# Performance work log

Measured on AMD Instinct MI355X. Metric: run time of the kernel, lower is better.

The kernel has to match this reference:

```python
import jax, jax.numpy as jnp
import numpy as np

B, T, C, H = 2, 2048, 1024, 16  # batch, seq, n_embd, n_head


def setup_inputs() -> dict:
    key = jax.random.key(0)
    k1, k2, k3 = jax.random.split(key, 3)
    scale = 0.02
    return {
        "x": jax.random.normal(k1, (B, T, C), dtype=jnp.float32),
        "W_attn": jax.random.normal(k2, (3 * C, C), dtype=jnp.float32) * scale,
        "b_attn": jnp.zeros((3 * C,), dtype=jnp.float32),
        "W_proj": jax.random.normal(k3, (C, C), dtype=jnp.float32) * scale,
        "b_proj": jnp.zeros((C,), dtype=jnp.float32),
        "alpha": jnp.asarray(1.0, dtype=jnp.float32),
        "beta": jnp.asarray(0.1, dtype=jnp.float32),
        "gamma": jnp.asarray(0.1, dtype=jnp.float32),
    }


def reference(x, W_attn, b_attn, W_proj, b_proj, alpha, beta, gamma):
    Bx, Tx, Cx = x.shape
    d = Cx // H  # head dim
    qkv = x @ W_attn.T + b_attn                      # [B,T,3C]
    q, k, v = jnp.split(qkv, 3, axis=-1)

    def to_heads(t):
        return t.reshape(Bx, Tx, H, d).transpose(0, 2, 1, 3)  # [B,H,T,d]

    q, k, v = to_heads(q), to_heads(k), to_heads(v)

    inv_sqrt_d = jnp.asarray(1.0 / np.sqrt(d), dtype=x.dtype)
    scores = jnp.einsum('bhtd,bhsd->bhts', q, k) * inv_sqrt_d  # [B,H,T,T]

    causal = jnp.tril(jnp.ones((Tx, Tx), dtype=bool))
    scores = jnp.where(causal, scores, -jnp.inf)
    att = jax.nn.softmax(scores, axis=-1)

    # Id buffer = softmax(10000*eye) == identity; MC buffer = softmax(10000*tril)
    # == uniform causal prefix average: MC[i, j<=i] = 1/(i+1).
    id_m = jnp.eye(Tx, dtype=x.dtype)
    mc = causal.astype(x.dtype) / jnp.arange(1, Tx + 1, dtype=x.dtype)[:, None]

    shaped = beta * att + alpha * id_m - gamma * mc  # dropout p=0 -> identity
    y = jnp.einsum('bhts,bhsd->bhtd', shaped, v)     # [B,H,T,d]
    y = y.transpose(0, 2, 1, 3).reshape(Bx, Tx, Cx)
    return y @ W_proj.T + b_proj
```

## Files before the change

### kernel.cpp

```cpp
#include <hip/hip_runtime.h>
#include <stdint.h>

#define Bsz  2
#define Tseq 2048
#define Cemb 1024
#define NH   16
#define HD   64

typedef __attribute__((ext_vector_type(8))) __bf16 bf16x8;
typedef __attribute__((ext_vector_type(4))) float  f32x4;
typedef __attribute__((ext_vector_type(8))) unsigned short u16x8;

#define MFMA16(a, b, c) __builtin_amdgcn_mfma_f32_16x16x32_bf16((a), (b), (c), 0, 0, 0)

__device__ __forceinline__ unsigned short f2bf(float f) {
  union { float f; unsigned int u; } v; v.f = f;
  unsigned int u = v.u;
  u += 0x7fffu + ((u >> 16) & 1u);
  return (unsigned short)(u >> 16);
}
__device__ __forceinline__ unsigned short f2bf_rhu(float f) {
  union { float f; unsigned int u; } v; v.f = f;
  return (unsigned short)((v.u + 0x8000u) >> 16);
}
__device__ __forceinline__ float bf2f(unsigned short h) {
  union { unsigned int u; float f; } v; v.u = ((unsigned int)h) << 16;
  return v.f;
}

typedef __attribute__((address_space(1))) const unsigned int GU;
typedef __attribute__((address_space(3))) unsigned int LU;
__device__ __forceinline__ void load_lds16(const void* g, void* l) {
  __builtin_amdgcn_global_load_lds((GU*)g, (LU*)l, 16, 0, 0);
}

__global__ void cast_bf16_kernel(const float* __restrict__ in,
                                 unsigned short* __restrict__ out, int n) {
  int i = (blockIdx.x * blockDim.x + threadIdx.x) * 4;
  if (i < n) {
    const float4 f = *(const float4*)(in + i);
    ushort4 o;
    o.x = f2bf(f.x); o.y = f2bf(f.y); o.z = f2bf(f.z); o.w = f2bf(f.w);
    *(ushort4*)(out + i) = o;
  }
}

__global__ __launch_bounds__(256) void gemm_qkv_kernel(
    const unsigned short* __restrict__ A,
    const unsigned short* __restrict__ Bw,
    const float* __restrict__ bias,
    unsigned short* __restrict__ qkv) {
  const int K = Cemb;
  __shared__ unsigned short sA[128 * 32];
  __shared__ unsigned short sB[128 * 32];
  const int tid = threadIdx.x;
  const int wave = tid >> 6, lane = tid & 63;
  const int quad = lane >> 4, lrow = lane & 15;
  const int l7 = lrow & 7;
  const int wm = (wave >> 1) * 64, wn = (wave & 1) * 64;
  const int tileM = blockIdx.y * 128, tileN = blockIdx.x * 128;

  f32x4 acc[4][4];
#pragma unroll
  for (int i = 0; i < 4; ++i)
#pragma unroll
    for (int j = 0; j < 4; ++j) acc[i][j] = (f32x4){0.f, 0.f, 0.f, 0.f};

  for (int k0 = 0; k0 < K; k0 += 32) {
    __syncthreads();
#pragma unroll
    for (int s = 0; s < 2; ++s) {
      const int cid = tid + s * 256;
      const int r = cid >> 2, ko = (cid & 3) * 8;
      load_lds16(&A[(size_t)(tileM + r) * K + k0 + ko], &sA[cid * 8]);
      load_lds16(&Bw[(size_t)(tileN + r) * K + k0 + ko], &sB[cid * 8]);
    }
    __syncthreads();
    bf16x8 af[4], bfm[4];
#pragma unroll
    for (int mt = 0; mt < 4; ++mt)
      af[mt] = *(const bf16x8*)&sA[(wm + mt * 16 + lrow) * 32 + quad * 8];
#pragma unroll
    for (int nt = 0; nt < 4; ++nt)
      bfm[nt] = *(const bf16x8*)&sB[(wn + nt * 16 + lrow) * 32 + quad * 8];
#pragma unroll
    for (int mt = 0; mt < 4; ++mt)
#pragma unroll
      for (int nt = 0; nt < 4; ++nt)
        acc[mt][nt] = MFMA16(af[mt], bfm[nt], acc[mt][nt]);
  }

  __syncthreads();
  unsigned short* sEp = sA + wave * 1024;
  float bias_v[4];
#pragma unroll
  for (int nt = 0; nt < 4; ++nt) bias_v[nt] = bias[tileN + wn + nt * 16 + lrow];
  const int gn0 = tileN + wn;
  const int part = gn0 >> 10, h = (gn0 & 1023) >> 6;

#pragma unroll
  for (int mt = 0; mt < 4; ++mt) {
#pragma unroll
    for (int nt = 0; nt < 4; ++nt)
#pragma unroll
      for (int reg = 0; reg < 4; ++reg) {
        const int q = quad * 4 + reg;
        const int ch = (nt * 2 + (lrow >> 3)) ^ (q & 7);
        sEp[q * 64 + ch * 8 + l7] = f2bf(acc[mt][nt][reg] + bias_v[nt]);
      }
    __builtin_amdgcn_wave_barrier();
#pragma unroll
    for (int i = 0; i < 2; ++i) {
      const int c = i * 64 + lane;
      const int r = c >> 3, ch2 = c & 7;
      const u16x8 row = *(const u16x8*)&sEp[r * 64 + ((ch2 ^ (r & 7)) << 3)];
      const int gm = tileM + wm + mt * 16 + r;
      const int bb = gm >> 11, t = gm & 2047;
      *(u16x8*)&qkv[((((size_t)part * Bsz + bb) * NH + h) * Tseq + t) * HD + ch2 * 8] = row;
    }
    __builtin_amdgcn_wave_barrier();
  }
}

__global__ __launch_bounds__(256) void gemm_proj_kernel(
    const unsigned short* __restrict__ A,
    const unsigned short* __restrict__ Bw,
    const float* __restrict__ bias,
    float* __restrict__ out) {
  const int K = Cemb;
  __shared__ unsigned short sA[128 * 32];
  __shared__ unsigned short sB[128 * 32];
  const int tid = threadIdx.x;
  const int wave = tid >> 6, lane = tid & 63;
  const int quad = lane >> 4, lrow = lane & 15;
  const int wm = (wave >> 1) * 64, wn = (wave & 1) * 64;
  const int tileM = blockIdx.y * 128, tileN = blockIdx.x * 128;

  f32x4 acc[4][4];
#pragma unroll
  for (int i = 0; i < 4; ++i)
#pragma unroll
    for (int j = 0; j < 4; ++j) acc[i][j] = (f32x4){0.f, 0.f, 0.f, 0.f};

  for (int k0 = 0; k0 < K; k0 += 32) {
    __syncthreads();
#pragma unroll
    for (int s = 0; s < 2; ++s) {
      const int cid = tid + s * 256;
      const int r = cid >> 2, ko = (cid & 3) * 8;
      load_lds16(&A[(size_t)(tileM + r) * K + k0 + ko], &sA[cid * 8]);
      load_lds16(&Bw[(size_t)(tileN + r) * K + k0 + ko], &sB[cid * 8]);
    }
    __syncthreads();
    bf16x8 af[4], bfm[4];
#pragma unroll
    for (int mt = 0; mt < 4; ++mt)
      af[mt] = *(const bf16x8*)&sA[(wm + mt * 16 + lrow) * 32 + quad * 8];
#pragma unroll
    for (int nt = 0; nt < 4; ++nt)
      bfm[nt] = *(const bf16x8*)&sB[(wn + nt * 16 + lrow) * 32 + quad * 8];
#pragma unroll
    for (int mt = 0; mt < 4; ++mt)
#pragma unroll
      for (int nt = 0; nt < 4; ++nt)
        acc[mt][nt] = MFMA16(af[mt], bfm[nt], acc[mt][nt]);
  }

#pragma unroll
  for (int mt = 0; mt < 4; ++mt)
#pragma unroll
    for (int nt = 0; nt < 4; ++nt)
#pragma unroll
      for (int reg = 0; reg < 4; ++reg) {
        const int gm = tileM + wm + mt * 16 + quad * 4 + reg;
        const int gn = tileN + wn + nt * 16 + lrow;
        out[(size_t)gm * Cemb + gn] = acc[mt][nt][reg] + bias[gn];
      }
}

__global__ __launch_bounds__(256) void attn_kernel(
    const unsigned short* __restrict__ qkv,
    const float* __restrict__ palpha, const float* __restrict__ pbeta,
    const float* __restrict__ pgamma,
    unsigned short* __restrict__ y) {
  __shared__ unsigned short sK[2][64 * 64];
  __shared__ unsigned short sVt[2][64 * 64];
  __shared__ unsigned short sP[2][4 * 16 * 64];

  const int tid = threadIdx.x;
  const int wave = tid >> 6, lane = tid & 63;
  const int quad = lane >> 4, lrow = lane & 15;
  const int l7 = lrow & 7;
  const int bh = blockIdx.y;
  const int b = bh >> 4, h = bh & 15;

  const size_t partStride = (size_t)Bsz * NH * Tseq * HD;
  const size_t headoff = (size_t)bh * Tseq * HD;
  const unsigned short* Q = qkv + headoff;
  const unsigned short* Kp = qkv + partStride + headoff;
  const unsigned short* Vp = qkv + 2 * partStride + headoff;

  const float alpha = palpha[0], beta = pbeta[0], gamma = pgamma[0];
  const float SCL = 0.125f * 1.44269504089f;

  union { unsigned short u[8]; bf16x8 v; } onesU;
#pragma unroll
  for (int j = 0; j < 8; ++j) onesU.u[j] = 0x3F80;
  const bf16x8 onesF = onesU.v;

  const int qtA = blockIdx.x;
  const int qtB = 31 - qtA;
  const int q0A = qtA * 64, q0B = qtB * 64;

  const int qrA = q0A + wave * 16 + lrow;
  const int qrB = q0B + wave * 16 + lrow;
  const bf16x8 aQA0 = *(const bf16x8*)&Q[(size_t)qrA * HD + quad * 8];
  const bf16x8 aQA1 = *(const bf16x8*)&Q[(size_t)qrA * HD + 32 + quad * 8];
  const bf16x8 aQB0 = *(const bf16x8*)&Q[(size_t)qrB * HD + quad * 8];
  const bf16x8 aQB1 = *(const bf16x8*)&Q[(size_t)qrB * HD + 32 + quad * 8];

  f32x4 OA[4], UA[4], OB[4], UB[4], LA, LB;
#pragma unroll
  for (int nt = 0; nt < 4; ++nt) {
    OA[nt] = (f32x4){0.f, 0.f, 0.f, 0.f};
    UA[nt] = (f32x4){0.f, 0.f, 0.f, 0.f};
    OB[nt] = (f32x4){0.f, 0.f, 0.f, 0.f};
    UB[nt] = (f32x4){0.f, 0.f, 0.f, 0.f};
  }
  LA = (f32x4){0.f, 0.f, 0.f, 0.f};
  LB = (f32x4){0.f, 0.f, 0.f, 0.f};

  const int kr0 = tid >> 3, kc0 = tid & 7;
  const int vd0 = (tid & 31) * 2;
  const int vrb = (tid >> 5) * 8;
  const int vch = tid >> 5;

  uint4 pk0, pk1;
  unsigned int pv[8];

  auto load_tile = [&](int it) {
    const int j0 = it * 64;
    pk0 = *(const uint4*)&Kp[(size_t)(j0 + kr0) * HD + kc0 * 8];
    pk1 = *(const uint4*)&Kp[(size_t)(j0 + 32 + kr0) * HD + kc0 * 8];
#pragma unroll
    for (int e = 0; e < 8; ++e)
      pv[e] = *(const unsigned int*)&Vp[(size_t)(j0 + vrb + e) * HD + vd0];
  };
  auto store_tile = [&](int buf) {
    unsigned short* K_ = sK[buf];
    unsigned short* Vt_ = sVt[buf];
    *(uint4*)&K_[kr0 * 64 + ((kc0 ^ (kr0 & 7)) << 3)] = pk0;
    const int r1 = 32 + kr0;
    *(uint4*)&K_[r1 * 64 + ((kc0 ^ (r1 & 7)) << 3)] = pk1;
    u16x8 lo, hi;
#pragma unroll
    for (int e = 0; e < 8; ++e) {
      lo[e] = (unsigned short)(pv[e] & 0xffffu);
      hi[e] = (unsigned short)(pv[e] >> 16);
    }
    *(u16x8*)&Vt_[vd0 * 64 + ((vch ^ (vd0 & 7)) << 3)] = lo;
    *(u16x8*)&Vt_[(vd0 + 1) * 64 + ((vch ^ ((vd0 + 1) & 7)) << 3)] = hi;
  };

  load_tile(0);
  store_tile(0);

  const int ntiles = qtB + 1;
  for (int it = 0; it < ntiles; ++it) {
    const int cur = it & 1;
    __syncthreads();
    if (it + 1 < ntiles) load_tile(it + 1);

    const unsigned short* K_ = sK[cur];
    const unsigned short* Vt_ = sVt[cur];
    const int j0 = it * 64;

    auto process = [&](const bf16x8& aQ0, const bf16x8& aQ1, f32x4* O, f32x4* U,
                       f32x4& L, int q0, int qt, unsigned short* sPt) {
      const bool diag = (it == qt);
      unsigned short* sPw = sPt + wave * 1024;
      float p[4][4];
#pragma unroll
      for (int ct = 0; ct < 4; ++ct) {
        const int kr = ct * 16 + lrow;
        const bf16x8 b0 = *(const bf16x8*)&K_[kr * 64 + ((quad ^ l7) << 3)];
        const bf16x8 b1 = *(const bf16x8*)&K_[kr * 64 + (((4 + quad) ^ l7) << 3)];
        f32x4 s = (f32x4){0.f, 0.f, 0.f, 0.f};
        s = MFMA16(aQ0, b0, s);
        s = MFMA16(aQ1, b1, s);
#pragma unroll
        for (int reg = 0; reg < 4; ++reg) {
          float v = s[reg] * SCL;
          if (diag) {
            const int qi = q0 + wave * 16 + quad * 4 + reg;
            const int kj = j0 + ct * 16 + lrow;
            if (kj > qi) v = -1e30f;
          }
          p[ct][reg] = exp2f(v);
        }
      }
#pragma unroll
      for (int ct = 0; ct < 4; ++ct)
#pragma unroll
        for (int reg = 0; reg < 4; ++reg) {
          const int q = quad * 4 + reg;
          sPw[q * 64 + (((ct * 2 + (lrow >> 3)) ^ (q & 7)) << 3) + l7] =
              f2bf_rhu(p[ct][reg]);
        }
      __builtin_amdgcn_wave_barrier();
      const bf16x8 aP0 = *(const bf16x8*)&sPw[lrow * 64 + ((quad ^ l7) << 3)];
      const bf16x8 aP1 = *(const bf16x8*)&sPw[lrow * 64 + (((4 + quad) ^ l7) << 3)];

      bf16x8 aOne0 = onesF, aOne1 = onesF;
      if (diag) {
        union { unsigned short u[8]; bf16x8 v; } m0, m1;
        const int qiu = q0 + wave * 16 + lrow;
#pragma unroll
        for (int jj = 0; jj < 8; ++jj) {
          m0.u[jj] = (j0 + quad * 8 + jj) <= qiu ? (unsigned short)0x3F80 : (unsigned short)0;
          m1.u[jj] = (j0 + 32 + quad * 8 + jj) <= qiu ? (unsigned short)0x3F80 : (unsigned short)0;
        }
        aOne0 = m0.v; aOne1 = m1.v;
      }

#pragma unroll
      for (int nt = 0; nt < 4; ++nt) {
        const int vr = nt * 16 + lrow;
        const bf16x8 bv0 = *(const bf16x8*)&Vt_[vr * 64 + ((quad ^ l7) << 3)];
        const bf16x8 bv1 = *(const bf16x8*)&Vt_[vr * 64 + (((4 + quad) ^ l7) << 3)];
        O[nt] = MFMA16(aP0, bv0, O[nt]);
        O[nt] = MFMA16(aP1, bv1, O[nt]);
        U[nt] = MFMA16(aOne0, bv0, U[nt]);
        U[nt] = MFMA16(aOne1, bv1, U[nt]);
      }
      L = MFMA16(aP0, onesF, L);
      L = MFMA16(aP1, onesF, L);
    };

    process(aQB0, aQB1, OB, UB, LB, q0B, qtB, sP[1]);
    if (it <= qtA) process(aQA0, aQA1, OA, UA, LA, q0A, qtA, sP[0]);

    if (it + 1 < ntiles) store_tile((it + 1) & 1);
  }

  auto epilogue = [&](const f32x4* O, const f32x4* U, const f32x4& L, int q0) {
#pragma unroll
    for (int reg = 0; reg < 4; ++reg) {
      const int qi = q0 + wave * 16 + quad * 4 + reg;
      const float bl = beta / L[reg];
      const float gi = gamma / (float)(qi + 1);
#pragma unroll
      for (int nt = 0; nt < 4; ++nt) {
        const int dd = nt * 16 + lrow;
        const float vv = bf2f(Vp[(size_t)qi * HD + dd]);
        const float yv = bl * O[nt][reg] + alpha * vv - gi * U[nt][reg];
        y[((size_t)b * Tseq + qi) * Cemb + h * HD + dd] = f2bf(yv);
      }
    }
  };
  epilogue(OA, UA, LA, q0A);
  epilogue(OB, UB, LB, q0B);
}

extern "C" void kernel_launch(void* const* d_in, const int* in_sizes, int n_in,
                              void* d_out, int out_size, void* d_ws, size_t ws_size,
                              hipStream_t stream) {
  const float* x  = (const float*)d_in[0];
  const float* Wa = (const float*)d_in[1];
  const float* ba = (const float*)d_in[2];
  const float* Wp = (const float*)d_in[3];
  const float* bp = (const float*)d_in[4];
  const float* alpha = (const float*)d_in[5];
  const float* beta  = (const float*)d_in[6];
  const float* gamma = (const float*)d_in[7];
  float* out = (float*)d_out;

  unsigned short* ws = (unsigned short*)d_ws;
  unsigned short* xb   = ws;
  unsigned short* wab  = xb + (size_t)4096 * 1024;
  unsigned short* wpb  = wab + (size_t)3072 * 1024;
  unsigned short* qkvb = wpb + (size_t)1024 * 1024;
  unsigned short* yb   = qkvb + (size_t)3 * Bsz * NH * Tseq * HD;

  {
    int n = 4096 * 1024;
    cast_bf16_kernel<<<(n / 4 + 255) / 256, 256, 0, stream>>>(x, xb, n);
    n = 3072 * 1024;
    cast_bf16_kernel<<<(n / 4 + 255) / 256, 256, 0, stream>>>(Wa, wab, n);
    n = 1024 * 1024;
    cast_bf16_kernel<<<(n / 4 + 255) / 256, 256, 0, stream>>>(Wp, wpb, n);
  }

  gemm_qkv_kernel<<<dim3(3072 / 128, 4096 / 128), 256, 0, stream>>>(xb, wab, ba, qkvb);
  attn_kernel<<<dim3(16, Bsz * NH), 256, 0, stream>>>(qkvb, alpha, beta, gamma, yb);
  gemm_proj_kernel<<<dim3(1024 / 128, 4096 / 128), 256, 0, stream>>>(yb, wpb, bp, out);
}
```

Before: 205.0 us.

## Deepen GEMM K-tiles, transpose attention to keep P in registers, one q-tile per block

Both GEMMs now stage 64-wide K slices with an XOR-swizzled LDS layout, which halves the number of barrier-separated load rounds. The attention kernel computes S transposed (K as the A operand, Q as B), so each lane's probabilities can be packed straight into the B operand for the PV MFMA. This drops the LDS round-trip for P and the sP buffer. It also switches from pairing two q-tiles per block to one q-tile per block with twice as many blocks and an occupancy hint of 4, trading the old load balancing for more parallelism and fewer registers.

```diff
diff --git a/kernel.cpp b/kernel.cpp
--- a/kernel.cpp
+++ b/kernel.cpp
@@ -19,13 +19,13 @@
   u += 0x7fffu + ((u >> 16) & 1u);
   return (unsigned short)(u >> 16);
 }
-__device__ __forceinline__ unsigned short f2bf_rhu(float f) {
-  union { float f; unsigned int u; } v; v.f = f;
-  return (unsigned short)((v.u + 0x8000u) >> 16);
-}
 __device__ __forceinline__ float bf2f(unsigned short h) {
   union { unsigned int u; float f; } v; v.u = ((unsigned int)h) << 16;
   return v.f;
+}
+__device__ __forceinline__ unsigned int pack_bf2(float a, float b) {
+  union { float f; unsigned int u; } va, vb; va.f = a; vb.f = b;
+  return __builtin_amdgcn_perm(vb.u + 0x8000u, va.u + 0x8000u, 0x07060302u);
 }
 
 typedef __attribute__((address_space(1))) const unsigned int GU;
@@ -51,8 +51,8 @@
     const float* __restrict__ bias,
     unsigned short* __restrict__ qkv) {
   const int K = Cemb;
-  __shared__ unsigned short sA[128 * 32];
-  __shared__ unsigned short sB[128 * 32];
+  __shared__ unsigned short sA[128 * 64];
+  __shared__ unsigned short sB[128 * 64];
   const int tid = threadIdx.x;
   const int wave = tid >> 6, lane = tid & 63;
   const int quad = lane >> 4, lrow = lane & 15;
@@ -66,28 +66,33 @@
 #pragma unroll
     for (int j = 0; j < 4; ++j) acc[i][j] = (f32x4){0.f, 0.f, 0.f, 0.f};
 
-  for (int k0 = 0; k0 < K; k0 += 32) {
-    __syncthreads();
-#pragma unroll
-    for (int s = 0; s < 2; ++s) {
+  for (int k0 = 0; k0 < K; k0 += 64) {
+    __syncthreads();
+#pragma unroll
+    for (int s = 0; s < 4; ++s) {
       const int cid = tid + s * 256;
-      const int r = cid >> 2, ko = (cid & 3) * 8;
-      load_lds16(&A[(size_t)(tileM + r) * K + k0 + ko], &sA[cid * 8]);
-      load_lds16(&Bw[(size_t)(tileN + r) * K + k0 + ko], &sB[cid * 8]);
-    }
-    __syncthreads();
-    bf16x8 af[4], bfm[4];
-#pragma unroll
-    for (int mt = 0; mt < 4; ++mt)
-      af[mt] = *(const bf16x8*)&sA[(wm + mt * 16 + lrow) * 32 + quad * 8];
-#pragma unroll
-    for (int nt = 0; nt < 4; ++nt)
-      bfm[nt] = *(const bf16x8*)&sB[(wn + nt * 16 + lrow) * 32 + quad * 8];
-#pragma unroll
-    for (int mt = 0; mt < 4; ++mt)
+      const int r = cid >> 3, c = (cid & 7) ^ (r & 7);
+      load_lds16(&A[(size_t)(tileM + r) * K + k0 + c * 8], &sA[cid * 8]);
+      load_lds16(&Bw[(size_t)(tileN + r) * K + k0 + c * 8], &sB[cid * 8]);
+    }
+    __syncthreads();
+#pragma unroll
+    for (int half = 0; half < 2; ++half) {
+      bf16x8 af[4], bfm[4];
+#pragma unroll
+      for (int mt = 0; mt < 4; ++mt)
+        af[mt] = *(const bf16x8*)&sA[(wm + mt * 16 + lrow) * 64 +
+                                     (((half * 4 + quad) ^ l7) << 3)];
 #pragma unroll
       for (int nt = 0; nt < 4; ++nt)
-        acc[mt][nt] = MFMA16(af[mt], bfm[nt], acc[mt][nt]);
+        bfm[nt] = *(const bf16x8*)&sB[(wn + nt * 16 + lrow) * 64 +
+                                      (((half * 4 + quad) ^ l7) << 3)];
+#pragma unroll
+      for (int mt = 0; mt < 4; ++mt)
+#pragma unroll
+        for (int nt = 0; nt < 4; ++nt)
+          acc[mt][nt] = MFMA16(af[mt], bfm[nt], acc[mt][nt]);
+    }
   }
 
   __syncthreads();
@@ -128,11 +133,12 @@
     const float* __restrict__ bias,
     float* __restrict__ out) {
   const int K = Cemb;
-  __shared__ unsigned short sA[128 * 32];
-  __shared__ unsigned short sB[128 * 32];
+  __shared__ unsigned short sA[128 * 64];
+  __shared__ unsigned short sB[128 * 64];
   const int tid = threadIdx.x;
   const int wave = tid >> 6, lane = tid & 63;
   const int quad = lane >> 4, lrow = lane & 15;
+  const int l7 = lrow & 7;
   const int wm = (wave >> 1) * 64, wn = (wave & 1) * 64;
   const int tileM = blockIdx.y * 128, tileN = blockIdx.x * 128;
 
@@ -142,28 +148,33 @@
 #pragma unroll
     for (int j = 0; j < 4; ++j) acc[i][j] = (f32x4){0.f, 0.f, 0.f, 0.f};
 
-  for (int k0 = 0; k0 < K; k0 += 32) {
-    __syncthreads();
-#pragma unroll
-    for (int s = 0; s < 2; ++s) {
+  for (int k0 = 0; k0 < K; k0 += 64) {
+    __syncthreads();
+#pragma unroll
+    for (int s = 0; s < 4; ++s) {
       const int cid = tid + s * 256;
-      const int r = cid >> 2, ko = (cid & 3) * 8;
-      load_lds16(&A[(size_t)(tileM + r) * K + k0 + ko], &sA[cid * 8]);
-      load_lds16(&Bw[(size_t)(tileN + r) * K + k0 + ko], &sB[cid * 8]);
-    }
-    __syncthreads();
-    bf16x8 af[4], bfm[4];
-#pragma unroll
-    for (int mt = 0; mt < 4; ++mt)
-      af[mt] = *(const bf16x8*)&sA[(wm + mt * 16 + lrow) * 32 + quad * 8];
-#pragma unroll
-    for (int nt = 0; nt < 4; ++nt)
-      bfm[nt] = *(const bf16x8*)&sB[(wn + nt * 16 + lrow) * 32 + quad * 8];
-#pragma unroll
-    for (int mt = 0; mt < 4; ++mt)
+      const int r = cid >> 3, c = (cid & 7) ^ (r & 7);
+      load_lds16(&A[(size_t)(tileM + r) * K + k0 + c * 8], &sA[cid * 8]);
+      load_lds16(&Bw[(size_t)(tileN + r) * K + k0 + c * 8], &sB[cid * 8]);
+    }
+    __syncthreads();
+#pragma unroll
+    for (int half = 0; half < 2; ++half) {
+      bf16x8 af[4], bfm[4];
+#pragma unroll
+      for (int mt = 0; mt < 4; ++mt)
+        af[mt] = *(const bf16x8*)&sA[(wm + mt * 16 + lrow) * 64 +
+                                     (((half * 4 + quad) ^ l7) << 3)];
 #pragma unroll
       for (int nt = 0; nt < 4; ++nt)
-        acc[mt][nt] = MFMA16(af[mt], bfm[nt], acc[mt][nt]);
+        bfm[nt] = *(const bf16x8*)&sB[(wn + nt * 16 + lrow) * 64 +
+                                      (((half * 4 + quad) ^ l7) << 3)];
+#pragma unroll
+      for (int mt = 0; mt < 4; ++mt)
+#pragma unroll
+        for (int nt = 0; nt < 4; ++nt)
+          acc[mt][nt] = MFMA16(af[mt], bfm[nt], acc[mt][nt]);
+    }
   }
 
 #pragma unroll
@@ -178,19 +189,17 @@
       }
 }
 
-__global__ __launch_bounds__(256) void attn_kernel(
+__global__ __launch_bounds__(256, 4) void attn_kernel(
     const unsigned short* __restrict__ qkv,
     const float* __restrict__ palpha, const float* __restrict__ pbeta,
     const float* __restrict__ pgamma,
     unsigned short* __restrict__ y) {
   __shared__ unsigned short sK[2][64 * 64];
   __shared__ unsigned short sVt[2][64 * 64];
-  __shared__ unsigned short sP[2][4 * 16 * 64];
 
   const int tid = threadIdx.x;
   const int wave = tid >> 6, lane = tid & 63;
   const int quad = lane >> 4, lrow = lane & 15;
-  const int l7 = lrow & 7;
   const int bh = blockIdx.y;
   const int b = bh >> 4, h = bh & 15;
 
@@ -208,32 +217,31 @@
   for (int j = 0; j < 8; ++j) onesU.u[j] = 0x3F80;
   const bf16x8 onesF = onesU.v;
 
-  const int qtA = blockIdx.x;
-  const int qtB = 31 - qtA;
-  const int q0A = qtA * 64, q0B = qtB * 64;
-
-  const int qrA = q0A + wave * 16 + lrow;
-  const int qrB = q0B + wave * 16 + lrow;
-  const bf16x8 aQA0 = *(const bf16x8*)&Q[(size_t)qrA * HD + quad * 8];
-  const bf16x8 aQA1 = *(const bf16x8*)&Q[(size_t)qrA * HD + 32 + quad * 8];
-  const bf16x8 aQB0 = *(const bf16x8*)&Q[(size_t)qrB * HD + quad * 8];
-  const bf16x8 aQB1 = *(const bf16x8*)&Q[(size_t)qrB * HD + 32 + quad * 8];
-
-  f32x4 OA[4], UA[4], OB[4], UB[4], LA, LB;
-#pragma unroll
-  for (int nt = 0; nt < 4; ++nt) {
-    OA[nt] = (f32x4){0.f, 0.f, 0.f, 0.f};
-    UA[nt] = (f32x4){0.f, 0.f, 0.f, 0.f};
-    OB[nt] = (f32x4){0.f, 0.f, 0.f, 0.f};
-    UB[nt] = (f32x4){0.f, 0.f, 0.f, 0.f};
-  }
-  LA = (f32x4){0.f, 0.f, 0.f, 0.f};
-  LB = (f32x4){0.f, 0.f, 0.f, 0.f};
+  const int qt = 31 - (int)blockIdx.x;
+  const int q0 = qt * 64;
+  const int ntiles = qt + 1;
+
+  const int qrow = q0 + wave * 16 + lrow;
+  const bf16x8 bQ0 = *(const bf16x8*)&Q[(size_t)qrow * HD + quad * 8];
+  const bf16x8 bQ1 = *(const bf16x8*)&Q[(size_t)qrow * HD + 32 + quad * 8];
+
+  const int prow = ((lrow & 12) << 1) | (lrow & 3);
+
+  f32x4 Ot[4], Ut[4], L;
+#pragma unroll
+  for (int dt = 0; dt < 4; ++dt) {
+    Ot[dt] = (f32x4){0.f, 0.f, 0.f, 0.f};
+    Ut[dt] = (f32x4){0.f, 0.f, 0.f, 0.f};
+  }
+  L = (f32x4){0.f, 0.f, 0.f, 0.f};
 
   const int kr0 = tid >> 3, kc0 = tid & 7;
+  const int hk = (kr0 & 7) ^ ((kr0 & 16) >> 2);
   const int vd0 = (tid & 31) * 2;
   const int vrb = (tid >> 5) * 8;
   const int vch = tid >> 5;
+  const int hv0 = (vd0 & 7) ^ ((vd0 & 16) >> 2);
+  const int hv1 = ((vd0 + 1) & 7) ^ (((vd0 + 1) & 16) >> 2);
 
   uint4 pk0, pk1;
   unsigned int pv[8];
@@ -249,23 +257,21 @@
   auto store_tile = [&](int buf) {
     unsigned short* K_ = sK[buf];
     unsigned short* Vt_ = sVt[buf];
-    *(uint4*)&K_[kr0 * 64 + ((kc0 ^ (kr0 & 7)) << 3)] = pk0;
-    const int r1 = 32 + kr0;
-    *(uint4*)&K_[r1 * 64 + ((kc0 ^ (r1 & 7)) << 3)] = pk1;
+    *(uint4*)&K_[kr0 * 64 + ((kc0 ^ hk) << 3)] = pk0;
+    *(uint4*)&K_[(32 + kr0) * 64 + ((kc0 ^ hk) << 3)] = pk1;
     u16x8 lo, hi;
 #pragma unroll
     for (int e = 0; e < 8; ++e) {
       lo[e] = (unsigned short)(pv[e] & 0xffffu);
       hi[e] = (unsigned short)(pv[e] >> 16);
     }
-    *(u16x8*)&Vt_[vd0 * 64 + ((vch ^ (vd0 & 7)) << 3)] = lo;
-    *(u16x8*)&Vt_[(vd0 + 1) * 64 + ((vch ^ ((vd0 + 1) & 7)) << 3)] = hi;
+    *(u16x8*)&Vt_[vd0 * 64 + ((vch ^ hv0) << 3)] = lo;
+    *(u16x8*)&Vt_[(vd0 + 1) * 64 + ((vch ^ hv1) << 3)] = hi;
   };
 
   load_tile(0);
   store_tile(0);
 
-  const int ntiles = qtB + 1;
   for (int it = 0; it < ntiles; ++it) {
     const int cur = it & 1;
     __syncthreads();
@@ -274,92 +280,86 @@
     const unsigned short* K_ = sK[cur];
     const unsigned short* Vt_ = sVt[cur];
     const int j0 = it * 64;
-
-    auto process = [&](const bf16x8& aQ0, const bf16x8& aQ1, f32x4* O, f32x4* U,
-                       f32x4& L, int q0, int qt, unsigned short* sPt) {
-      const bool diag = (it == qt);
-      unsigned short* sPw = sPt + wave * 1024;
-      float p[4][4];
-#pragma unroll
-      for (int ct = 0; ct < 4; ++ct) {
-        const int kr = ct * 16 + lrow;
-        const bf16x8 b0 = *(const bf16x8*)&K_[kr * 64 + ((quad ^ l7) << 3)];
-        const bf16x8 b1 = *(const bf16x8*)&K_[kr * 64 + (((4 + quad) ^ l7) << 3)];
-        f32x4 s = (f32x4){0.f, 0.f, 0.f, 0.f};
-        s = MFMA16(aQ0, b0, s);
-        s = MFMA16(aQ1, b1, s);
+    const bool diag = (it == qt);
+
+    unsigned int pk2[4][2];
+#pragma unroll
+    for (int ct = 0; ct < 4; ++ct) {
+      const int srow = (ct >> 1) * 32 + (ct & 1) * 4 + prow;
+      const int hs = (srow & 7) ^ ((srow & 16) >> 2);
+      const bf16x8 a0 = *(const bf16x8*)&K_[srow * 64 + ((quad ^ hs) << 3)];
+      const bf16x8 a1 = *(const bf16x8*)&K_[srow * 64 + (((4 + quad) ^ hs) << 3)];
+      f32x4 s = (f32x4){0.f, 0.f, 0.f, 0.f};
+      s = MFMA16(a0, bQ0, s);
+      s = MFMA16(a1, bQ1, s);
+      float p[4];
+      if (diag) {
+        const int sbase = j0 + (ct >> 1) * 32 + (ct & 1) * 4 + quad * 8;
 #pragma unroll
         for (int reg = 0; reg < 4; ++reg) {
-          float v = s[reg] * SCL;
-          if (diag) {
-            const int qi = q0 + wave * 16 + quad * 4 + reg;
-            const int kj = j0 + ct * 16 + lrow;
-            if (kj > qi) v = -1e30f;
-          }
-          p[ct][reg] = exp2f(v);
+          const float v = (sbase + reg > qrow) ? -1e30f : s[reg] * SCL;
+          p[reg] = exp2f(v);
         }
+      } else {
+#pragma unroll
+        for (int reg = 0; reg < 4; ++reg) p[reg] = exp2f(s[reg] * SCL);
       }
-#pragma unroll
-      for (int ct = 0; ct < 4; ++ct)
-#pragma unroll
-        for (int reg = 0; reg < 4; ++reg) {
-          const int q = quad * 4 + reg;
-          sPw[q * 64 + (((ct * 2 + (lrow >> 3)) ^ (q & 7)) << 3) + l7] =
-              f2bf_rhu(p[ct][reg]);
-        }
-      __builtin_amdgcn_wave_barrier();
-      const bf16x8 aP0 = *(const bf16x8*)&sPw[lrow * 64 + ((quad ^ l7) << 3)];
-      const bf16x8 aP1 = *(const bf16x8*)&sPw[lrow * 64 + (((4 + quad) ^ l7) << 3)];
-
-      bf16x8 aOne0 = onesF, aOne1 = onesF;
-      if (diag) {
-        union { unsigned short u[8]; bf16x8 v; } m0, m1;
-        const int qiu = q0 + wave * 16 + lrow;
-#pragma unroll
-        for (int jj = 0; jj < 8; ++jj) {
-          m0.u[jj] = (j0 + quad * 8 + jj) <= qiu ? (unsigned short)0x3F80 : (unsigned short)0;
-          m1.u[jj] = (j0 + 32 + quad * 8 + jj) <= qiu ? (unsigned short)0x3F80 : (unsigned short)0;
-        }
-        aOne0 = m0.v; aOne1 = m1.v;
+      pk2[ct][0] = pack_bf2(p[0], p[1]);
+      pk2[ct][1] = pack_bf2(p[2], p[3]);
+    }
+    union { unsigned int w[4]; bf16x8 v; } P1u, P2u;
+    P1u.w[0] = pk2[0][0]; P1u.w[1] = pk2[0][1];
+    P1u.w[2] = pk2[1][0]; P1u.w[3] = pk2[1][1];
+    P2u.w[0] = pk2[2][0]; P2u.w[1] = pk2[2][1];
+    P2u.w[2] = pk2[3][0]; P2u.w[3] = pk2[3][1];
+    const bf16x8 P1 = P1u.v, P2 = P2u.v;
+
+    L = MFMA16(onesF, P1, L);
+    L = MFMA16(onesF, P2, L);
+
+    bf16x8 u1 = onesF, u2 = onesF;
+    if (diag) {
+      union { unsigned short u[8]; bf16x8 v; } m0, m1;
+#pragma unroll
+      for (int jj = 0; jj < 8; ++jj) {
+        m0.u[jj] = (j0 + quad * 8 + jj) <= qrow ? (unsigned short)0x3F80 : (unsigned short)0;
+        m1.u[jj] = (j0 + 32 + quad * 8 + jj) <= qrow ? (unsigned short)0x3F80 : (unsigned short)0;
       }
-
-#pragma unroll
-      for (int nt = 0; nt < 4; ++nt) {
-        const int vr = nt * 16 + lrow;
-        const bf16x8 bv0 = *(const bf16x8*)&Vt_[vr * 64 + ((quad ^ l7) << 3)];
-        const bf16x8 bv1 = *(const bf16x8*)&Vt_[vr * 64 + (((4 + quad) ^ l7) << 3)];
-        O[nt] = MFMA16(aP0, bv0, O[nt]);
-        O[nt] = MFMA16(aP1, bv1, O[nt]);
-        U[nt] = MFMA16(aOne0, bv0, U[nt]);
-        U[nt] = MFMA16(aOne1, bv1, U[nt]);
-      }
-      L = MFMA16(aP0, onesF, L);
-      L = MFMA16(aP1, onesF, L);
-    };
-
-    process(aQB0, aQB1, OB, UB, LB, q0B, qtB, sP[1]);
-    if (it <= qtA) process(aQA0, aQA1, OA, UA, LA, q0A, qtA, sP[0]);
+      u1 = m0.v; u2 = m1.v;
+    }
+
+#pragma unroll
+    for (int dt = 0; dt < 4; ++dt) {
+      const int vr = dt * 16 + lrow;
+      const int hvr = (vr & 7) ^ ((vr & 16) >> 2);
+      const bf16x8 av0 = *(const bf16x8*)&Vt_[vr * 64 + ((quad ^ hvr) << 3)];
+      const bf16x8 av1 = *(const bf16x8*)&Vt_[vr * 64 + (((4 + quad) ^ hvr) << 3)];
+      Ot[dt] = MFMA16(av0, P1, Ot[dt]);
+      Ot[dt] = MFMA16(av1, P2, Ot[dt]);
+      Ut[dt] = MFMA16(av0, u1, Ut[dt]);
+      Ut[dt] = MFMA16(av1, u2, Ut[dt]);
+    }
 
     if (it + 1 < ntiles) store_tile((it + 1) & 1);
   }
 
-  auto epilogue = [&](const f32x4* O, const f32x4* U, const f32x4& L, int q0) {
+  const float bl = beta / L[0];
+  const float gi = gamma / (float)(qrow + 1);
+  const size_t ybase = ((size_t)b * Tseq + qrow) * Cemb + h * HD;
+#pragma unroll
+  for (int dt = 0; dt < 4; ++dt) {
+    const int d0 = dt * 16 + quad * 4;
+    const ushort4 vv4 = *(const ushort4*)&Vp[(size_t)qrow * HD + d0];
+    const unsigned short vu[4] = {vv4.x, vv4.y, vv4.z, vv4.w};
+    ushort4 o;
+    unsigned short* op = (unsigned short*)&o;
 #pragma unroll
     for (int reg = 0; reg < 4; ++reg) {
-      const int qi = q0 + wave * 16 + quad * 4 + reg;
-      const float bl = beta / L[reg];
-      const float gi = gamma / (float)(qi + 1);
-#pragma unroll
-      for (int nt = 0; nt < 4; ++nt) {
-        const int dd = nt * 16 + lrow;
-        const float vv = bf2f(Vp[(size_t)qi * HD + dd]);
-        const float yv = bl * O[nt][reg] + alpha * vv - gi * U[nt][reg];
-        y[((size_t)b * Tseq + qi) * Cemb + h * HD + dd] = f2bf(yv);
-      }
-    }
-  };
-  epilogue(OA, UA, LA, q0A);
-  epilogue(OB, UB, LB, q0B);
+      const float yv = bl * Ot[dt][reg] + alpha * bf2f(vu[reg]) - gi * Ut[dt][reg];
+      op[reg] = f2bf(yv);
+    }
+    *(ushort4*)&y[ybase + d0] = o;
+  }
 }
 
 extern "C" void kernel_launch(void* const* d_in, const int* in_sizes, int n_in,
@@ -392,6 +392,6 @@
   }
 
   gemm_qkv_kernel<<<dim3(3072 / 128, 4096 / 128), 256, 0, stream>>>(xb, wab, ba, qkvb);
-  attn_kernel<<<dim3(16, Bsz * NH), 256, 0, stream>>>(qkvb, alpha, beta, gamma, yb);
+  attn_kernel<<<dim3(32, Bsz * NH), 256, 0, stream>>>(qkvb, alpha, beta, gamma, yb);
   gemm_proj_kernel<<<dim3(1024 / 128, 4096 / 128), 256, 0, stream>>>(yb, wpb, bp, out);
 }
```

Measured after the change: 227.4 us. +10.9%, slower.
